# Kernel optimization log

Measured on AMD Instinct MI355X. Metric: run time of the kernel, lower is better.

The kernel has to match this reference:

```python
import jax, jax.numpy as jnp
import numpy as np

NUM_HEADS = 16
HIDDEN = 1024
HEAD_DIM = HIDDEN // NUM_HEADS
B, S, D = 2, 2048, 1024


def setup_inputs() -> dict:
    key = jax.random.key(0)
    ks = jax.random.split(key, 7)
    scale = 1.0 / np.sqrt(D)
    return {
        "query": jax.random.normal(ks[0], (B, S, D), dtype=jnp.float32),
        "key": jax.random.normal(ks[1], (B, S, D), dtype=jnp.float32),
        "value": jax.random.normal(ks[2], (B, S, D), dtype=jnp.float32),
        "Wk_w": jax.random.normal(ks[3], (HIDDEN, D), dtype=jnp.float32) * scale,
        "Wk_b": jax.random.normal(ks[4], (HIDDEN,), dtype=jnp.float32) * scale,
        "Wv_w": jax.random.normal(ks[5], (HIDDEN, D), dtype=jnp.float32) * scale,
        "Wv_b": jax.random.normal(ks[6], (HIDDEN,), dtype=jnp.float32) * scale,
    }


def reference(query, key, value, Wk_w, Wk_b, Wv_w, Wv_b):
    # NOTE: in the original torch module, self.W_v is assigned twice, so the
    # SAME Linear (Wv) projects both key and value; Wk projects query.
    b, s, _ = query.shape

    def split_heads(x):  # [b,s,hidden] -> [b,h,s,hd]
        return x.reshape(b, s, NUM_HEADS, HEAD_DIM).transpose(0, 2, 1, 3)

    q = split_heads(query @ Wk_w.T + Wk_b)
    k = split_heads(key @ Wv_w.T + Wv_b)
    v = split_heads(value @ Wv_w.T + Wv_b)

    scores = jnp.einsum("bhqd,bhkd->bhqk", q, k) / jnp.sqrt(
        jnp.asarray(HEAD_DIM, dtype=q.dtype))
    probs = jax.nn.softmax(scores, axis=-1)
    out = jnp.einsum("bhqk,bhkd->bhqd", probs, v)
    return out.transpose(0, 2, 1, 3).reshape(b, s, NUM_HEADS * HEAD_DIM)
```

## Files before the change

kernel.cpp:

```cpp
#include <hip/hip_runtime.h>
#include <stdint.h>

typedef unsigned short u16;
typedef uint32_t u32;
typedef __bf16 bf16x8 __attribute__((ext_vector_type(8)));
typedef float f32x4 __attribute__((ext_vector_type(4)));
typedef u16 u16x4 __attribute__((ext_vector_type(4)));
typedef u16 u16x8 __attribute__((ext_vector_type(8)));

#define XQ_OFF 0ul
#define XK_OFF 4194304ul
#define XV_OFF 8388608ul
#define WK_OFF 12582912ul
#define WV_OFF 13631488ul
#define Q_OFF  14680064ul
#define K_OFF  18874368ul
#define V_OFF  23068672ul

#define SCQ 0.18033688011112042f

__device__ __forceinline__ u16 f2bf(float f) {
  u32 u = __float_as_uint(f);
  u32 r = (u + 0x7fffu + ((u >> 16) & 1u)) >> 16;
  return (u16)r;
}

__device__ __forceinline__ u32 pk2(float a, float b) {
  typedef __bf16 bf2_t __attribute__((ext_vector_type(2)));
  typedef float f2_t __attribute__((ext_vector_type(2)));
  f2_t v; v[0] = a; v[1] = b;
  bf2_t h = __builtin_convertvector(v, bf2_t);
  union { bf2_t h; u32 u; } cv; cv.h = h; return cv.u;
}

__device__ __forceinline__ void load_lds16(const void* g, void* l) {
  __builtin_amdgcn_global_load_lds(
      (const __attribute__((address_space(1))) u32*)g,
      (__attribute__((address_space(3))) u32*)l, 16, 0, 0);
}

__global__ __launch_bounds__(256) void cvt_tile_kernel(
    const float* __restrict__ xq, const float* __restrict__ xk,
    const float* __restrict__ xv, const float* __restrict__ wk,
    const float* __restrict__ wv, u16* __restrict__ ws) {
  __shared__ u16 tile[4096];
  const int bid = blockIdx.x;
  const float* src; size_t dstbase; int rt, ktp;
  if (bid < 3072) {
    int m = bid >> 10, loc = bid & 1023;
    src = (m == 0) ? xq : (m == 1) ? xk : xv;
    dstbase = (size_t)m * 4194304ul;
    rt = loc >> 4; ktp = loc & 15;
  } else {
    int r2 = bid - 3072;
    int m = r2 >> 8, loc = r2 & 255;
    src = m ? wv : wk;
    dstbase = WK_OFF + (size_t)m * 1048576ul;
    rt = loc >> 4; ktp = loc & 15;
  }
  const int t = threadIdx.x;
  const int row = t >> 2, kq = (t & 3) << 4;
  const float* s = src + (size_t)(rt * 64 + row) * 1024ul + ktp * 64 + kq;
#pragma unroll
  for (int i = 0; i < 4; ++i) {
    float4 v = *(const float4*)(s + i * 4);
    int k = kq + i * 4;
    u32* p = (u32*)(tile + ((k >> 5) * 2048 + ((k >> 3) & 3) * 512 + row * 8 + (k & 7)));
    p[0] = pk2(v.x, v.y);
    p[1] = pk2(v.z, v.w);
  }
  __syncthreads();
  u16* dst = ws + dstbase + (size_t)(rt * 32 + ktp * 2) * 2048ul;
#pragma unroll
  for (int so = 0; so < 4096; so += 2048)
    *(u16x8*)(dst + so + t * 8) = *(const u16x8*)(tile + so + t * 8);
}

__global__ __launch_bounds__(256) void proj_kernel(u16* __restrict__ ws,
                                                   const float* __restrict__ bk,
                                                   const float* __restrict__ bv) {
  const int proj = blockIdx.z;
  const int mtile = blockIdx.y;
  const int ntile = blockIdx.x;
  const u16* A = ws + (size_t)proj * 4194304ul;
  const u16* Bw = ws + ((proj == 0) ? WK_OFF : WV_OFF);
  const float* bias = (proj == 0) ? bk : bv;
  u16* outQ = ws + Q_OFF;
  u16* outK = ws + K_OFF;
  u16* outV = ws + V_OFF;

  __shared__ u16 As[8192];
  __shared__ u16 Bs[8192];

  const int t = threadIdx.x;
  const int w = t >> 6, lane = t & 63, g = lane >> 4, c = lane & 15;
  const int wm = w >> 1, wn = w & 1;

  f32x4 acc[4][4];
#pragma unroll
  for (int mt = 0; mt < 4; ++mt)
#pragma unroll
    for (int nt = 0; nt < 4; ++nt) acc[mt][nt] = (f32x4){0.f, 0.f, 0.f, 0.f};

  const int off = t * 16;
#pragma unroll 1
  for (int kk = 0; kk < 16; ++kk) {
    const char* Ag = (const char*)(A + (size_t)mtile * 131072ul + (size_t)kk * 4096ul);
    const char* Bg = (const char*)(Bw + (size_t)ntile * 131072ul + (size_t)kk * 4096ul);
    load_lds16(Ag + off, (char*)As + off);
    load_lds16(Ag + off + 4096, (char*)As + off + 4096);
    load_lds16(Ag + 131072 + off, (char*)As + 8192 + off);
    load_lds16(Ag + 131072 + off + 4096, (char*)As + 8192 + off + 4096);
    load_lds16(Bg + off, (char*)Bs + off);
    load_lds16(Bg + off + 4096, (char*)Bs + off + 4096);
    load_lds16(Bg + 131072 + off, (char*)Bs + 8192 + off);
    load_lds16(Bg + 131072 + off + 4096, (char*)Bs + 8192 + off + 4096);
    __syncthreads();
#pragma unroll
    for (int kc = 0; kc < 2; ++kc) {
      bf16x8 af[4], bf[4];
#pragma unroll
      for (int mt = 0; mt < 4; ++mt)
        af[mt] = *(const bf16x8*)(As + wm * 4096 + kc * 2048 + g * 512 + (mt * 16 + c) * 8);
#pragma unroll
      for (int nt = 0; nt < 4; ++nt)
        bf[nt] = *(const bf16x8*)(Bs + wn * 4096 + kc * 2048 + g * 512 + (nt * 16 + c) * 8);
#pragma unroll
      for (int mt = 0; mt < 4; ++mt)
#pragma unroll
        for (int nt = 0; nt < 4; ++nt)
          acc[mt][nt] = __builtin_amdgcn_mfma_f32_16x16x32_bf16(af[mt], bf[nt], acc[mt][nt], 0, 0, 0);
    }
    __syncthreads();
  }

  const int m0 = mtile * 128 + wm * 64, n0 = ntile * 128 + wn * 64;
#pragma unroll
  for (int nt = 0; nt < 4; ++nt) {
    const int col = n0 + nt * 16 + c;
    const float bvv = bias[col];
    const int h = col >> 6, d = col & 63;
#pragma unroll
    for (int mt = 0; mt < 4; ++mt) {
      const int mbase = m0 + mt * 16 + g * 4;
      const int b = mbase >> 11;
      const int bh = b * 16 + h;
      if (proj == 2) {
        const int s = mbase & 2047;
        u16x4 pk;
#pragma unroll
        for (int r = 0; r < 4; ++r) pk[r] = f2bf(acc[mt][nt][r] + bvv);
        size_t idx = (size_t)bh * 131072ul + (size_t)(s >> 6) * 4096ul +
                     (size_t)((s & 63) >> 3) * 512ul + (size_t)d * 8ul + (size_t)(s & 7);
        *(u16x4*)(outV + idx) = pk;
      } else {
        u16* dst = (proj == 0) ? outQ : outK;
#pragma unroll
        for (int r = 0; r < 4; ++r) {
          const int m = mbase + r;
          const int s = m & 2047;
          float y = acc[mt][nt][r] + bvv;
          if (proj == 0) y *= SCQ;
          size_t idx;
          if (proj == 0)
            idx = (size_t)bh * 131072ul + (size_t)(s >> 7) * 8192ul + (size_t)(d >> 3) * 1024ul +
                  (size_t)(s & 127) * 8ul + (size_t)(d & 7);
          else
            idx = (size_t)bh * 131072ul + (size_t)(s >> 6) * 4096ul + (size_t)(d >> 3) * 512ul +
                  (size_t)(s & 63) * 8ul + (size_t)(d & 7);
          dst[idx] = f2bf(y);
        }
      }
    }
  }
}

__global__ __launch_bounds__(256, 4) void attn_kernel(const u16* __restrict__ ws,
                                                      float* __restrict__ out) {
  const int qtile = blockIdx.x, bh = blockIdx.y, half = blockIdx.z;
  const int b = bh >> 4, h = bh & 15;
  const int t = threadIdx.x, w = t >> 6, lane = t & 63, g = lane >> 4, c = lane & 15;

  __shared__ u16 Ks[4096];
  __shared__ u16 Vs[4096];
  __shared__ __align__(16) u16 Ps[9216];

  const u16* Qg = ws + Q_OFF + (size_t)bh * 131072ul + (size_t)qtile * 8192ul;
  const u16* Kg = ws + K_OFF + (size_t)bh * 131072ul + (size_t)half * 65536ul;
  const u16* Vg = ws + V_OFF + (size_t)bh * 131072ul + (size_t)half * 65536ul;
  float* Opart = (float*)ws;
  float* Lh = ((float*)ws) + 4194304ul + (size_t)half * 65536ul;

  const int off = t * 16;
  load_lds16((const char*)Kg + off, (char*)Ks + off);
  load_lds16((const char*)Kg + off + 4096, (char*)Ks + off + 4096);
  load_lds16((const char*)Vg + off, (char*)Vs + off);
  load_lds16((const char*)Vg + off + 4096, (char*)Vs + off + 4096);

  bf16x8 qf[2][2];
#pragma unroll
  for (int mtq = 0; mtq < 2; ++mtq)
#pragma unroll
    for (int ks = 0; ks < 2; ++ks)
      qf[mtq][ks] = *(const bf16x8*)(Qg + (ks * 4 + g) * 1024 + (w * 32 + mtq * 16 + c) * 8);

  u16x8 ou;
  const u16 one = (c == 0) ? (u16)0x3F80 : (u16)0;
#pragma unroll
  for (int i = 0; i < 8; ++i) ou[i] = one;
  union { u16x8 u; bf16x8 b; } ocv; ocv.u = ou;
  const bf16x8 onesf = ocv.b;

  f32x4 O[2][4], Lacc[2];
#pragma unroll
  for (int mtq = 0; mtq < 2; ++mtq) {
    Lacc[mtq] = (f32x4){0.f, 0.f, 0.f, 0.f};
#pragma unroll
    for (int nt = 0; nt < 4; ++nt) O[mtq][nt] = (f32x4){0.f, 0.f, 0.f, 0.f};
  }

  __syncthreads();
  u16* Psw = Ps + w * 2304;

#pragma unroll 1
  for (int j = 0; j < 16; ++j) {
    f32x4 St[4][2];
#pragma unroll
    for (int mtk = 0; mtk < 4; ++mtk)
#pragma unroll
      for (int ntq = 0; ntq < 2; ++ntq) St[mtk][ntq] = (f32x4){0.f, 0.f, 0.f, 0.f};
#pragma unroll
    for (int ks = 0; ks < 2; ++ks) {
      bf16x8 kf[4];
#pragma unroll
      for (int mtk = 0; mtk < 4; ++mtk)
        kf[mtk] = *(const bf16x8*)(Ks + (ks * 4 + g) * 512 + (mtk * 16 + c) * 8);
#pragma unroll
      for (int mtk = 0; mtk < 4; ++mtk)
#pragma unroll
        for (int ntq = 0; ntq < 2; ++ntq)
          St[mtk][ntq] =
              __builtin_amdgcn_mfma_f32_16x16x32_bf16(kf[mtk], qf[ntq][ks], St[mtk][ntq], 0, 0, 0);
    }
#pragma unroll
    for (int mtk = 0; mtk < 4; ++mtk)
#pragma unroll
      for (int ntq = 0; ntq < 2; ++ntq)
#pragma unroll
        for (int r = 0; r < 4; ++r) St[mtk][ntq][r] = exp2f(St[mtk][ntq][r]);
#pragma unroll
    for (int ntq = 0; ntq < 2; ++ntq)
#pragma unroll
      for (int mtk = 0; mtk < 4; ++mtk) {
        u32 lo = pk2(St[mtk][ntq][0], St[mtk][ntq][1]);
        u32 hi = pk2(St[mtk][ntq][2], St[mtk][ntq][3]);
        u32* p = (u32*)(Psw + (ntq * 16 + c) * 72 + mtk * 16 + g * 4);
        p[0] = lo; p[1] = hi;
      }
    asm volatile("s_waitcnt lgkmcnt(0)" ::: "memory");
#pragma unroll
    for (int ks = 0; ks < 2; ++ks) {
      bf16x8 pf[2], vf[4];
#pragma unroll
      for (int mtq = 0; mtq < 2; ++mtq)
        pf[mtq] = *(const bf16x8*)(Psw + (mtq * 16 + c) * 72 + ks * 32 + g * 8);
#pragma unroll
      for (int nt = 0; nt < 4; ++nt)
        vf[nt] = *(const bf16x8*)(Vs + (ks * 4 + g) * 512 + (nt * 16 + c) * 8);
#pragma unroll
      for (int mtq = 0; mtq < 2; ++mtq) {
        Lacc[mtq] = __builtin_amdgcn_mfma_f32_16x16x32_bf16(pf[mtq], onesf, Lacc[mtq], 0, 0, 0);
#pragma unroll
        for (int nt = 0; nt < 4; ++nt)
          O[mtq][nt] = __builtin_amdgcn_mfma_f32_16x16x32_bf16(pf[mtq], vf[nt], O[mtq][nt], 0, 0, 0);
      }
    }
    __syncthreads();
    if (j < 15) {
      const char* Kj = (const char*)(Kg + (size_t)(j + 1) * 4096ul);
      const char* Vj = (const char*)(Vg + (size_t)(j + 1) * 4096ul);
      load_lds16(Kj + off, (char*)Ks + off);
      load_lds16(Kj + off + 4096, (char*)Ks + off + 4096);
      load_lds16(Vj + off, (char*)Vs + off);
      load_lds16(Vj + off + 4096, (char*)Vs + off + 4096);
      __syncthreads();
    }
  }

  float* Odst = half ? Opart : out;
  const int q0 = qtile * 128 + w * 32;
#pragma unroll
  for (int mtq = 0; mtq < 2; ++mtq)
#pragma unroll
    for (int r = 0; r < 4; ++r) {
      const int q = q0 + mtq * 16 + g * 4 + r;
      float* rowp = Odst + (size_t)(b * 2048 + q) * 1024ul + h * 64;
#pragma unroll
      for (int nt = 0; nt < 4; ++nt) rowp[nt * 16 + c] = O[mtq][nt][r];
    }
  if (c == 0) {
#pragma unroll
    for (int mtq = 0; mtq < 2; ++mtq)
#pragma unroll
      for (int r = 0; r < 4; ++r)
        Lh[(size_t)bh * 2048ul + q0 + mtq * 16 + g * 4 + r] = Lacc[mtq][r];
  }
}

__global__ __launch_bounds__(256) void combine_kernel(float* __restrict__ out,
                                                      const float* __restrict__ wsf) {
  const int tid = blockIdx.x * 256 + threadIdx.x;
  const int fl = tid << 2;
  const int q = (fl >> 10) & 2047, b = fl >> 21, h = (fl >> 6) & 15;
  const int bh = b * 16 + h;
  const float* L0 = wsf + 4194304ul;
  const float* L1 = wsf + 4194304ul + 65536ul;
  const float l = L0[bh * 2048 + q] + L1[bh * 2048 + q];
  const float inv = 1.0f / l;
  float4 o = *(float4*)(out + fl);
  const float4 p = *(const float4*)(wsf + fl);
  o.x = (o.x + p.x) * inv;
  o.y = (o.y + p.y) * inv;
  o.z = (o.z + p.z) * inv;
  o.w = (o.w + p.w) * inv;
  *(float4*)(out + fl) = o;
}

extern "C" void kernel_launch(void* const* d_in, const int* in_sizes, int n_in,
                              void* d_out, int out_size, void* d_ws, size_t ws_size,
                              hipStream_t stream) {
  const float* q = (const float*)d_in[0];
  const float* k = (const float*)d_in[1];
  const float* v = (const float*)d_in[2];
  const float* wk = (const float*)d_in[3];
  const float* bk = (const float*)d_in[4];
  const float* wv = (const float*)d_in[5];
  const float* bv = (const float*)d_in[6];
  u16* ws = (u16*)d_ws;
  float* out = (float*)d_out;

  cvt_tile_kernel<<<3584, 256, 0, stream>>>(q, k, v, wk, wv, ws);
  proj_kernel<<<dim3(8, 32, 3), 256, 0, stream>>>(ws, bk, bv);
  attn_kernel<<<dim3(16, 32, 2), 256, 0, stream>>>(ws, out);
  combine_kernel<<<4096, 256, 0, stream>>>(out, (const float*)ws);
}
```

Measured before the change: 214.0 us.

## Double-buffer GEMM and attention tiles, drop split-KV combine, coalesce conversion loads

```diff
diff --git a/kernel.cpp b/kernel.cpp
--- a/kernel.cpp
+++ b/kernel.cpp
@@ -18,6 +18,12 @@
 #define V_OFF  23068672ul
 
 #define SCQ 0.18033688011112042f
+
+#if __has_builtin(__builtin_amdgcn_exp2f)
+#define EXP2F(x) __builtin_amdgcn_exp2f(x)
+#else
+#define EXP2F(x) exp2f(x)
+#endif
 
 __device__ __forceinline__ u16 f2bf(float f) {
   u32 u = __float_as_uint(f);
@@ -59,12 +65,13 @@
     rt = loc >> 4; ktp = loc & 15;
   }
   const int t = threadIdx.x;
-  const int row = t >> 2, kq = (t & 3) << 4;
-  const float* s = src + (size_t)(rt * 64 + row) * 1024ul + ktp * 64 + kq;
+  const int row0 = t >> 4, c = t & 15;
+  const int k = c * 4;
+  const float* s = src + (size_t)(rt * 64 + row0) * 1024ul + ktp * 64 + k;
 #pragma unroll
   for (int i = 0; i < 4; ++i) {
-    float4 v = *(const float4*)(s + i * 4);
-    int k = kq + i * 4;
+    float4 v = *(const float4*)(s + (size_t)i * 16384ul);
+    int row = row0 + i * 16;
     u32* p = (u32*)(tile + ((k >> 5) * 2048 + ((k >> 3) & 3) * 512 + row * 8 + (k & 7)));
     p[0] = pk2(v.x, v.y);
     p[1] = pk2(v.z, v.w);
@@ -89,12 +96,16 @@
   u16* outK = ws + K_OFF;
   u16* outV = ws + V_OFF;
 
-  __shared__ u16 As[8192];
-  __shared__ u16 Bs[8192];
+  __shared__ u16 As[2][4096];
+  __shared__ u16 Bs[2][4096];
 
   const int t = threadIdx.x;
   const int w = t >> 6, lane = t & 63, g = lane >> 4, c = lane & 15;
   const int wm = w >> 1, wn = w & 1;
+  const int off = t * 16;
+
+  const char* Ag = (const char*)(A + (size_t)(2 * mtile) * 65536ul);
+  const char* Bg = (const char*)(Bw + (size_t)(2 * ntile) * 65536ul);
 
   f32x4 acc[4][4];
 #pragma unroll
@@ -102,35 +113,39 @@
 #pragma unroll
     for (int nt = 0; nt < 4; ++nt) acc[mt][nt] = (f32x4){0.f, 0.f, 0.f, 0.f};
 
-  const int off = t * 16;
+  load_lds16(Ag + off, (char*)As[0] + off);
+  load_lds16(Ag + 131072 + off, (char*)As[0] + 4096 + off);
+  load_lds16(Bg + off, (char*)Bs[0] + off);
+  load_lds16(Bg + 131072 + off, (char*)Bs[0] + 4096 + off);
+  __syncthreads();
+
 #pragma unroll 1
-  for (int kk = 0; kk < 16; ++kk) {
-    const char* Ag = (const char*)(A + (size_t)mtile * 131072ul + (size_t)kk * 4096ul);
-    const char* Bg = (const char*)(Bw + (size_t)ntile * 131072ul + (size_t)kk * 4096ul);
-    load_lds16(Ag + off, (char*)As + off);
-    load_lds16(Ag + off + 4096, (char*)As + off + 4096);
-    load_lds16(Ag + 131072 + off, (char*)As + 8192 + off);
-    load_lds16(Ag + 131072 + off + 4096, (char*)As + 8192 + off + 4096);
-    load_lds16(Bg + off, (char*)Bs + off);
-    load_lds16(Bg + off + 4096, (char*)Bs + off + 4096);
-    load_lds16(Bg + 131072 + off, (char*)Bs + 8192 + off);
-    load_lds16(Bg + 131072 + off + 4096, (char*)Bs + 8192 + off + 4096);
-    __syncthreads();
-#pragma unroll
-    for (int kc = 0; kc < 2; ++kc) {
-      bf16x8 af[4], bf[4];
-#pragma unroll
-      for (int mt = 0; mt < 4; ++mt)
-        af[mt] = *(const bf16x8*)(As + wm * 4096 + kc * 2048 + g * 512 + (mt * 16 + c) * 8);
+  for (int kk = 0; kk < 32; ++kk) {
+    const int cur = kk & 1;
+    if (kk < 31) {
+      const char* An = Ag + (size_t)(kk + 1) * 4096ul;
+      const char* Bn = Bg + (size_t)(kk + 1) * 4096ul;
+      char* Ad = (char*)As[cur ^ 1];
+      char* Bd = (char*)Bs[cur ^ 1];
+      load_lds16(An + off, Ad + off);
+      load_lds16(An + 131072 + off, Ad + 4096 + off);
+      load_lds16(Bn + off, Bd + off);
+      load_lds16(Bn + 131072 + off, Bd + 4096 + off);
+    }
+    const u16* Ac = As[cur];
+    const u16* Bc = Bs[cur];
+    bf16x8 af[4], bf[4];
+#pragma unroll
+    for (int mt = 0; mt < 4; ++mt)
+      af[mt] = *(const bf16x8*)(Ac + wm * 2048 + g * 512 + (mt * 16 + c) * 8);
+#pragma unroll
+    for (int nt = 0; nt < 4; ++nt)
+      bf[nt] = *(const bf16x8*)(Bc + wn * 2048 + g * 512 + (nt * 16 + c) * 8);
+#pragma unroll
+    for (int mt = 0; mt < 4; ++mt)
 #pragma unroll
       for (int nt = 0; nt < 4; ++nt)
-        bf[nt] = *(const bf16x8*)(Bs + wn * 4096 + kc * 2048 + g * 512 + (nt * 16 + c) * 8);
-#pragma unroll
-      for (int mt = 0; mt < 4; ++mt)
-#pragma unroll
-        for (int nt = 0; nt < 4; ++nt)
-          acc[mt][nt] = __builtin_amdgcn_mfma_f32_16x16x32_bf16(af[mt], bf[nt], acc[mt][nt], 0, 0, 0);
-    }
+        acc[mt][nt] = __builtin_amdgcn_mfma_f32_16x16x32_bf16(af[mt], bf[nt], acc[mt][nt], 0, 0, 0);
     __syncthreads();
   }
 
@@ -175,39 +190,36 @@
   }
 }
 
-__global__ __launch_bounds__(256, 4) void attn_kernel(const u16* __restrict__ ws,
+__global__ __launch_bounds__(256, 2) void attn_kernel(const u16* __restrict__ ws,
                                                       float* __restrict__ out) {
-  const int qtile = blockIdx.x, bh = blockIdx.y, half = blockIdx.z;
+  const int qtile = blockIdx.x, bh = blockIdx.y;
   const int b = bh >> 4, h = bh & 15;
   const int t = threadIdx.x, w = t >> 6, lane = t & 63, g = lane >> 4, c = lane & 15;
 
-  __shared__ u16 Ks[4096];
-  __shared__ u16 Vs[4096];
-  __shared__ __align__(16) u16 Ps[9216];
+  __shared__ u16 Ks[2][4096];
+  __shared__ u16 Vs[2][4096];
+  __shared__ __align__(16) u16 Ps[4][1280];
 
   const u16* Qg = ws + Q_OFF + (size_t)bh * 131072ul + (size_t)qtile * 8192ul;
-  const u16* Kg = ws + K_OFF + (size_t)bh * 131072ul + (size_t)half * 65536ul;
-  const u16* Vg = ws + V_OFF + (size_t)bh * 131072ul + (size_t)half * 65536ul;
-  float* Opart = (float*)ws;
-  float* Lh = ((float*)ws) + 4194304ul + (size_t)half * 65536ul;
+  const u16* Kg = ws + K_OFF + (size_t)bh * 131072ul;
+  const u16* Vg = ws + V_OFF + (size_t)bh * 131072ul;
 
   const int off = t * 16;
-  load_lds16((const char*)Kg + off, (char*)Ks + off);
-  load_lds16((const char*)Kg + off + 4096, (char*)Ks + off + 4096);
-  load_lds16((const char*)Vg + off, (char*)Vs + off);
-  load_lds16((const char*)Vg + off + 4096, (char*)Vs + off + 4096);
+  load_lds16((const char*)Kg + off, (char*)Ks[0] + off);
+  load_lds16((const char*)Kg + 4096 + off, (char*)Ks[0] + 4096 + off);
+  load_lds16((const char*)Vg + off, (char*)Vs[0] + off);
+  load_lds16((const char*)Vg + 4096 + off, (char*)Vs[0] + 4096 + off);
 
   bf16x8 qf[2][2];
 #pragma unroll
-  for (int mtq = 0; mtq < 2; ++mtq)
+  for (int ntq = 0; ntq < 2; ++ntq)
 #pragma unroll
     for (int ks = 0; ks < 2; ++ks)
-      qf[mtq][ks] = *(const bf16x8*)(Qg + (ks * 4 + g) * 1024 + (w * 32 + mtq * 16 + c) * 8);
+      qf[ntq][ks] = *(const bf16x8*)(Qg + (ks * 4 + g) * 1024 + (w * 32 + ntq * 16 + c) * 8);
 
   u16x8 ou;
-  const u16 one = (c == 0) ? (u16)0x3F80 : (u16)0;
-#pragma unroll
-  for (int i = 0; i < 8; ++i) ou[i] = one;
+#pragma unroll
+  for (int i = 0; i < 8; ++i) ou[i] = (u16)0x3F80;
   union { u16x8 u; bf16x8 b; } ocv; ocv.u = ou;
   const bf16x8 onesf = ocv.b;
 
@@ -219,11 +231,25 @@
     for (int nt = 0; nt < 4; ++nt) O[mtq][nt] = (f32x4){0.f, 0.f, 0.f, 0.f};
   }
 
+  u16* Psw = Ps[w];
   __syncthreads();
-  u16* Psw = Ps + w * 2304;
 
 #pragma unroll 1
-  for (int j = 0; j < 16; ++j) {
+  for (int j = 0; j < 32; ++j) {
+    const int cur = j & 1;
+    if (j < 31) {
+      const char* Kn = (const char*)(Kg + (size_t)(j + 1) * 4096ul);
+      const char* Vn = (const char*)(Vg + (size_t)(j + 1) * 4096ul);
+      char* Kd = (char*)Ks[cur ^ 1];
+      char* Vd = (char*)Vs[cur ^ 1];
+      load_lds16(Kn + off, Kd + off);
+      load_lds16(Kn + 4096 + off, Kd + 4096 + off);
+      load_lds16(Vn + off, Vd + off);
+      load_lds16(Vn + 4096 + off, Vd + 4096 + off);
+    }
+    const u16* Kc = Ks[cur];
+    const u16* Vc = Vs[cur];
+
     f32x4 St[4][2];
 #pragma unroll
     for (int mtk = 0; mtk < 4; ++mtk)
@@ -234,7 +260,7 @@
       bf16x8 kf[4];
 #pragma unroll
       for (int mtk = 0; mtk < 4; ++mtk)
-        kf[mtk] = *(const bf16x8*)(Ks + (ks * 4 + g) * 512 + (mtk * 16 + c) * 8);
+        kf[mtk] = *(const bf16x8*)(Kc + (ks * 4 + g) * 512 + (mtk * 16 + c) * 8);
 #pragma unroll
       for (int mtk = 0; mtk < 4; ++mtk)
 #pragma unroll
@@ -247,26 +273,27 @@
 #pragma unroll
       for (int ntq = 0; ntq < 2; ++ntq)
 #pragma unroll
-        for (int r = 0; r < 4; ++r) St[mtk][ntq][r] = exp2f(St[mtk][ntq][r]);
-#pragma unroll
-    for (int ntq = 0; ntq < 2; ++ntq)
-#pragma unroll
-      for (int mtk = 0; mtk < 4; ++mtk) {
-        u32 lo = pk2(St[mtk][ntq][0], St[mtk][ntq][1]);
-        u32 hi = pk2(St[mtk][ntq][2], St[mtk][ntq][3]);
-        u32* p = (u32*)(Psw + (ntq * 16 + c) * 72 + mtk * 16 + g * 4);
-        p[0] = lo; p[1] = hi;
-      }
-    asm volatile("s_waitcnt lgkmcnt(0)" ::: "memory");
-#pragma unroll
-    for (int ks = 0; ks < 2; ++ks) {
+        for (int r = 0; r < 4; ++r) St[mtk][ntq][r] = EXP2F(St[mtk][ntq][r]);
+#pragma unroll
+    for (int ksh = 0; ksh < 2; ++ksh) {
+#pragma unroll
+      for (int ntq = 0; ntq < 2; ++ntq)
+#pragma unroll
+        for (int m2 = 0; m2 < 2; ++m2) {
+          const int mtk = ksh * 2 + m2;
+          u32 lo = pk2(St[mtk][ntq][0], St[mtk][ntq][1]);
+          u32 hi = pk2(St[mtk][ntq][2], St[mtk][ntq][3]);
+          u32* p = (u32*)(Psw + (ntq * 16 + c) * 40 + m2 * 16 + g * 4);
+          p[0] = lo; p[1] = hi;
+        }
+      asm volatile("s_waitcnt lgkmcnt(0)" ::: "memory");
       bf16x8 pf[2], vf[4];
 #pragma unroll
       for (int mtq = 0; mtq < 2; ++mtq)
-        pf[mtq] = *(const bf16x8*)(Psw + (mtq * 16 + c) * 72 + ks * 32 + g * 8);
+        pf[mtq] = *(const bf16x8*)(Psw + (mtq * 16 + c) * 40 + g * 8);
 #pragma unroll
       for (int nt = 0; nt < 4; ++nt)
-        vf[nt] = *(const bf16x8*)(Vs + (ks * 4 + g) * 512 + (nt * 16 + c) * 8);
+        vf[nt] = *(const bf16x8*)(Vc + (ksh * 4 + g) * 512 + (nt * 16 + c) * 8);
 #pragma unroll
       for (int mtq = 0; mtq < 2; ++mtq) {
         Lacc[mtq] = __builtin_amdgcn_mfma_f32_16x16x32_bf16(pf[mtq], onesf, Lacc[mtq], 0, 0, 0);
@@ -276,54 +303,19 @@
       }
     }
     __syncthreads();
-    if (j < 15) {
-      const char* Kj = (const char*)(Kg + (size_t)(j + 1) * 4096ul);
-      const char* Vj = (const char*)(Vg + (size_t)(j + 1) * 4096ul);
-      load_lds16(Kj + off, (char*)Ks + off);
-      load_lds16(Kj + off + 4096, (char*)Ks + off + 4096);
-      load_lds16(Vj + off, (char*)Vs + off);
-      load_lds16(Vj + off + 4096, (char*)Vs + off + 4096);
-      __syncthreads();
-    }
-  }
-
-  float* Odst = half ? Opart : out;
+  }
+
   const int q0 = qtile * 128 + w * 32;
 #pragma unroll
   for (int mtq = 0; mtq < 2; ++mtq)
 #pragma unroll
     for (int r = 0; r < 4; ++r) {
+      const float inv = 1.0f / Lacc[mtq][r];
       const int q = q0 + mtq * 16 + g * 4 + r;
-      float* rowp = Odst + (size_t)(b * 2048 + q) * 1024ul + h * 64;
-#pragma unroll
-      for (int nt = 0; nt < 4; ++nt) rowp[nt * 16 + c] = O[mtq][nt][r];
-    }
-  if (c == 0) {
-#pragma unroll
-    for (int mtq = 0; mtq < 2; ++mtq)
-#pragma unroll
-      for (int r = 0; r < 4; ++r)
-        Lh[(size_t)bh * 2048ul + q0 + mtq * 16 + g * 4 + r] = Lacc[mtq][r];
-  }
-}
-
-__global__ __launch_bounds__(256) void combine_kernel(float* __restrict__ out,
-                                                      const float* __restrict__ wsf) {
-  const int tid = blockIdx.x * 256 + threadIdx.x;
-  const int fl = tid << 2;
-  const int q = (fl >> 10) & 2047, b = fl >> 21, h = (fl >> 6) & 15;
-  const int bh = b * 16 + h;
-  const float* L0 = wsf + 4194304ul;
-  const float* L1 = wsf + 4194304ul + 65536ul;
-  const float l = L0[bh * 2048 + q] + L1[bh * 2048 + q];
-  const float inv = 1.0f / l;
-  float4 o = *(float4*)(out + fl);
-  const float4 p = *(const float4*)(wsf + fl);
-  o.x = (o.x + p.x) * inv;
-  o.y = (o.y + p.y) * inv;
-  o.z = (o.z + p.z) * inv;
-  o.w = (o.w + p.w) * inv;
-  *(float4*)(out + fl) = o;
+      float* rowp = out + (size_t)(b * 2048 + q) * 1024ul + h * 64;
+#pragma unroll
+      for (int nt = 0; nt < 4; ++nt) rowp[nt * 16 + c] = O[mtq][nt][r] * inv;
+    }
 }
 
 extern "C" void kernel_launch(void* const* d_in, const int* in_sizes, int n_in,
@@ -341,6 +333,5 @@
 
   cvt_tile_kernel<<<3584, 256, 0, stream>>>(q, k, v, wk, wv, ws);
   proj_kernel<<<dim3(8, 32, 3), 256, 0, stream>>>(ws, bk, bv);
-  attn_kernel<<<dim3(16, 32, 2), 256, 0, stream>>>(ws, out);
-  combine_kernel<<<4096, 256, 0, stream>>>(out, (const float*)ws);
-}
+  attn_kernel<<<dim3(16, 32), 256, 0, stream>>>(ws, out);
+}
```

New measurement: 200.9 us. 1.07x faster.
